# Kernel tuning notes

Hardware: AMD Instinct MI355X
Metric: run time of the kernel (lower is better)

## Reference

```python
import jax, jax.numpy as jnp
import numpy as np

B, T, HID = 2, 2048, 3840
H, KV, D = 16, 8, 256
EPS = 1e-6
WINDOW = 1024
THETA_LOCAL = 10000.0
THETA_GLOBAL = 1000000.0


def _rope_tables(theta, t, d):
    inv_freq = 1.0 / (theta ** (jnp.arange(0, d, 2, dtype=jnp.float32) / d))  # (d/2,)
    ang = jnp.arange(t, dtype=jnp.float32)[:, None] * inv_freq[None, :]        # (T, d/2)
    return jnp.cos(ang), jnp.sin(ang)


def setup_inputs() -> dict:
    key = jax.random.key(0)
    ks = jax.random.split(key, 8)
    x = jax.random.normal(ks[0], (B, T, HID), dtype=jnp.float32)
    wq = jax.random.normal(ks[1], (H * D, HID), dtype=jnp.float32) * 0.02
    wk = jax.random.normal(ks[2], (KV * D, HID), dtype=jnp.float32) * 0.02
    wv = jax.random.normal(ks[3], (KV * D, HID), dtype=jnp.float32) * 0.02
    wo = jax.random.normal(ks[4], (HID, H * D), dtype=jnp.float32) * 0.02
    q_norm_w = 1.0 + jax.random.normal(ks[5], (D,), dtype=jnp.float32) * 0.02
    k_norm_w = 1.0 + jax.random.normal(ks[6], (D,), dtype=jnp.float32) * 0.02
    cos_g, sin_g = _rope_tables(THETA_GLOBAL, T, D)
    cos_l, sin_l = _rope_tables(THETA_LOCAL, T, D)
    # causal + sliding-window(1024) additive float mask, shape (1,1,T,T)
    i = jnp.arange(T)[:, None]
    j = jnp.arange(T)[None, :]
    allowed = (j <= i) & (i - j < WINDOW)
    attention_mask = jnp.where(allowed, 0.0, -1e9).astype(jnp.float32)[None, None]
    return {"x": x, "cos_global": cos_g, "sin_global": sin_g, "cos_local": cos_l,
            "sin_local": sin_l, "attention_mask": attention_mask,
            "wq": wq, "wk": wk, "wv": wv, "wo": wo,
            "q_norm_w": q_norm_w, "k_norm_w": k_norm_w}


def _rms_norm(x, w):
    # add=False variant: x * rsqrt(mean(x^2)+eps) * w, computed in fp32
    norm = jax.lax.rsqrt(jnp.mean(jnp.square(x), axis=-1, keepdims=True) + EPS)
    return x * norm * w


def _apply_rope(x, cos, sin):
    # x: (B, H, T, D); cos/sin: (T, D/2)
    t = x.shape[2]
    c = cos[:t][None, None]
    s = sin[:t][None, None]
    x1, x2 = x[..., : x.shape[-1] // 2], x[..., x.shape[-1] // 2 :]
    return jnp.concatenate([x1 * c - x2 * s, x2 * c + x1 * s], axis=-1)


def reference(x, cos_global, sin_global, cos_local, sin_local, attention_mask,
              wq, wk, wv, wo, q_norm_w, k_norm_w):
    b, t, _ = x.shape
    q = (x @ wq.T).reshape(b, t, H, D).transpose(0, 2, 1, 3)   # (B,H,T,D)
    k = (x @ wk.T).reshape(b, t, KV, D).transpose(0, 2, 1, 3)  # (B,KV,T,D)
    v = (x @ wv.T).reshape(b, t, KV, D).transpose(0, 2, 1, 3)
    q = _rms_norm(q, q_norm_w)
    k = _rms_norm(k, k_norm_w)
    # layer_idx=0 -> sliding-window layer -> local rope
    q = _apply_rope(q, cos_local, sin_local)
    k = _apply_rope(k, cos_local, sin_local)
    rep = H // KV
    k = jnp.repeat(k, rep, axis=1)  # repeat_interleave over head dim
    v = jnp.repeat(v, rep, axis=1)
    scale = 1.0 / jnp.sqrt(jnp.float32(D))
    scores = jnp.einsum("bhqd,bhkd->bhqk", q, k) * scale + attention_mask
    attn = jax.nn.softmax(scores, axis=-1)
    out = jnp.einsum("bhqk,bhkd->bhqd", attn, v)
    out = out.transpose(0, 2, 1, 3).reshape(b, t, H * D)
    return out @ wo.T
```

## Files before the change

### kernel.cpp

```cpp
#include <hip/hip_runtime.h>
#include <hip/hip_bf16.h>

typedef __hip_bfloat16 BF;
typedef __attribute__((ext_vector_type(8))) short short8;
typedef __attribute__((ext_vector_type(4))) float f32x4;

#define DEV __device__ __forceinline__

DEV void gll16(const BF* g, BF* l) {
  __builtin_amdgcn_global_load_lds(
      (const __attribute__((address_space(1))) void*)g,
      (__attribute__((address_space(3))) void*)l, 16, 0, 0);
}

DEV unsigned short bfbits(float f) {
  BF b = __float2bfloat16(f);
  return *reinterpret_cast<unsigned short*>(&b);
}

__global__ void f32_to_bf16_k(const float* __restrict__ in, BF* __restrict__ out, int n4) {
  int i = blockIdx.x * blockDim.x + threadIdx.x;
  if (i >= n4) return;
  const float4 v = ((const float4*)in)[i];
  ((ushort4*)out)[i] = make_ushort4(bfbits(v.x), bfbits(v.y), bfbits(v.z), bfbits(v.w));
}

__global__ void f32_to_bf16_pad_k(const float* __restrict__ in, BF* __restrict__ out, int n4) {
  int i = blockIdx.x * blockDim.x + threadIdx.x;
  if (i >= n4) return;
  const float4 v = ((const float4*)in)[i];
  const int r = i >> 10;
  const int c = i & 1023;
  ((ushort4*)out)[r * 1040 + c] = make_ushort4(bfbits(v.x), bfbits(v.y), bfbits(v.z), bfbits(v.w));
}

#define PHASE(MH, KK, READB, STAGE, TAIL)                                            \
  {                                                                                  \
    short8 af[4];                                                                    \
    const BF* Ap = Ax + (KK)*8192;                                                   \
    _Pragma("unroll") for (int m = 0; m < 4; ++m)                                    \
        af[m] = *(const short8*)&Ap[(wm*128 + (MH)*64 + m*16 + l15) * 32 + rd8];     \
    if (READB) {                                                                     \
      const BF* Bp = Bx + (KK)*8192;                                                 \
      _Pragma("unroll") for (int n = 0; n < 4; ++n)                                  \
          breg[n] = *(const short8*)&Bp[(wn*64 + n*16 + l15) * 32 + rd8];            \
    }                                                                                \
    STAGE                                                                            \
    __builtin_amdgcn_s_barrier();                                                    \
    asm volatile("s_waitcnt lgkmcnt(0)" ::: "memory");                               \
    __builtin_amdgcn_sched_barrier(0);                                               \
    __builtin_amdgcn_s_setprio(1);                                                   \
    _Pragma("unroll") for (int m = 0; m < 4; ++m)                                    \
      _Pragma("unroll") for (int n = 0; n < 4; ++n)                                  \
        acc[(MH)*4 + m][n] =                                                         \
            __builtin_amdgcn_mfma_f32_16x16x32_bf16(af[m], breg[n], acc[(MH)*4+m][n], 0, 0, 0); \
    __builtin_amdgcn_s_setprio(0);                                                   \
    TAIL                                                                             \
    __builtin_amdgcn_s_barrier();                                                    \
  }

template <typename CT>
DEV void gemm256_body(const BF* __restrict__ A, const BF* __restrict__ Bm,
                      CT* __restrict__ C, const int M, const int N, const int K,
                      const int lda, const int ldb) {
  extern __shared__ __align__(16) BF lds[];
  BF* ldsA = lds;
  BF* ldsB = lds + 32768;
  const int ntl = N >> 8;
  const int mtl = M >> 8;
  int mt, nt;
  if (mtl == 16 && ntl == 32) {
    const int x = blockIdx.x & 7;
    const int c = blockIdx.x >> 3;
    mt = ((x >> 2) << 3) + (c >> 3);
    nt = ((x & 3) << 3) + (c & 7);
  } else {
    const int cpx = gridDim.x >> 3;
    const int swzb = (blockIdx.x & 7) * cpx + (blockIdx.x >> 3);
    mt = swzb / ntl;
    nt = swzb % ntl;
  }
  const int m0 = mt << 8, n0 = nt << 8;
  const int tid = threadIdx.x, lane = tid & 63, w = tid >> 6;
  const int l15 = lane & 15, g = lane >> 4;
  const int wm = w >> 2, wn = w & 3;
  const int rd8 = (g ^ ((l15 >> 1) & 3)) << 3;
  const int trow = tid >> 2;
  const int scol = ((lane & 3) ^ ((lane >> 3) & 3)) << 3;
  const BF* aS = A + (size_t)(m0 + trow) * lda + scol;
  const BF* bS = Bm + (size_t)(n0 + trow) * ldb + scol;
  const size_t rstpA = (size_t)128 * lda;
  const size_t rstpB = (size_t)128 * ldb;
  BF* dA = ldsA + w * 512;
  BF* dB = ldsB + w * 512;
  const int NT = K >> 6;

  f32x4 acc[8][4];
#pragma unroll
  for (int m = 0; m < 8; ++m)
#pragma unroll
    for (int n = 0; n < 4; ++n) acc[m][n] = (f32x4){0.f, 0.f, 0.f, 0.f};
  short8 breg[4];

#define STG2(SRC, RST, DST) { gll16((SRC), (DST)); gll16((SRC) + (RST), (DST) + 4096); }

  STG2(aS, rstpA, dA);
  STG2(bS, rstpB, dB);
  STG2(aS + 32, rstpA, dA + 8192);
  STG2(bS + 32, rstpB, dB + 8192);
  STG2(aS + 64, rstpA, dA + 16384);
  STG2(bS + 64, rstpB, dB + 16384);
  asm volatile("s_waitcnt vmcnt(8)" ::: "memory");
  __builtin_amdgcn_sched_barrier(0);
  __builtin_amdgcn_s_barrier();

  for (int t = 0; t < NT; ++t) {
    const int bX = (t & 1) << 14;
    const int bY = bX ^ 16384;
    const BF* Ax = ldsA + bX;
    const BF* Bx = ldsB + bX;
    const int kc1 = (t + 1) << 6, kc2 = (t + 2) << 6;
    const bool s1 = (t + 1 < NT), s2 = (t + 2 < NT);
    PHASE(0, 0, 1, if (s1) STG2(aS + kc1 + 32, rstpA, dA + bY + 8192);, )
    PHASE(1, 0, 0, if (s1) STG2(bS + kc1 + 32, rstpB, dB + bY + 8192);,
          { asm volatile("s_waitcnt vmcnt(8)" ::: "memory");
            __builtin_amdgcn_sched_barrier(0); } )
    PHASE(0, 1, 1, if (s2) STG2(aS + kc2, rstpA, dA + bX);, )
    PHASE(1, 1, 0, if (s2) STG2(bS + kc2, rstpB, dB + bX);,
          if (s2) { asm volatile("s_waitcnt vmcnt(8)" ::: "memory");
                    __builtin_amdgcn_sched_barrier(0); }
          else    { asm volatile("s_waitcnt vmcnt(0)" ::: "memory");
                    __builtin_amdgcn_sched_barrier(0); } )
  }

#pragma unroll
  for (int mi = 0; mi < 8; ++mi) {
    const int gr = m0 + wm * 128 + mi * 16 + g * 4;
#pragma unroll
    for (int n = 0; n < 4; ++n) {
      const int gc = n0 + wn * 64 + n * 16 + l15;
#pragma unroll
      for (int r = 0; r < 4; ++r) {
        const float v = acc[mi][n][r];
        if constexpr (sizeof(CT) == 2)
          C[(size_t)(gr + r) * N + gc] = __float2bfloat16(v);
        else
          C[(size_t)(gr + r) * N + gc] = v;
      }
    }
  }
}

__global__ __launch_bounds__(512, 2) void gemm_qkv(const BF* __restrict__ A,
                                                   const BF* __restrict__ Bm,
                                                   BF* __restrict__ C,
                                                   int M, int N, int K, int lda, int ldb) {
  gemm256_body<BF>(A, Bm, C, M, N, K, lda, ldb);
}
__global__ __launch_bounds__(512, 2) void gemm_out(const BF* __restrict__ A,
                                                   const BF* __restrict__ Bm,
                                                   float* __restrict__ C,
                                                   int M, int N, int K, int lda, int ldb) {
  gemm256_body<float>(A, Bm, C, M, N, K, lda, ldb);
}

__global__ __launch_bounds__(256) void rmsrope(const BF* __restrict__ C1,
                                               BF* __restrict__ Qo, BF* __restrict__ Ko,
                                               const float* __restrict__ cosl,
                                               const float* __restrict__ sinl,
                                               const float* __restrict__ qw,
                                               const float* __restrict__ kw) {
  const int gwid = (blockIdx.x * 256 + threadIdx.x) >> 6;
  const int lane = threadIdx.x & 63;
  const int slot = gwid % 24;
  const int bt = gwid / 24;
  const int b = bt >> 11, t = bt & 2047;
  const BF* src;
  BF* dst;
  const float* wgt;
  if (slot < 16) {
    src = C1 + (size_t)bt * 8192 + slot * 256;
    dst = Qo + ((size_t)(b * 16 + slot) * 2048 + t) * 256;
    wgt = qw;
  } else {
    const int kv = slot - 16;
    src = C1 + (size_t)bt * 8192 + 4096 + kv * 256;
    dst = Ko + ((size_t)(b * 8 + kv) * 2048 + t) * 256;
    wgt = kw;
  }
  const int d2 = lane * 2;
  const ushort2 lo = *(const ushort2*)((const unsigned short*)src + d2);
  const ushort2 hi = *(const ushort2*)((const unsigned short*)src + 128 + d2);
  float x0 = __bfloat162float(*(const BF*)&lo.x);
  float x1 = __bfloat162float(*(const BF*)&lo.y);
  float x2 = __bfloat162float(*(const BF*)&hi.x);
  float x3 = __bfloat162float(*(const BF*)&hi.y);
  float ss = x0 * x0 + x1 * x1 + x2 * x2 + x3 * x3;
#pragma unroll
  for (int mm = 32; mm >= 1; mm >>= 1) ss += __shfl_xor(ss, mm);
  const float nrm = rsqrtf(ss * (1.f / 256.f) + 1e-6f);
  const float2 wlo = *(const float2*)(wgt + d2);
  const float2 whi = *(const float2*)(wgt + 128 + d2);
  x0 *= nrm * wlo.x;
  x1 *= nrm * wlo.y;
  x2 *= nrm * whi.x;
  x3 *= nrm * whi.y;
  const float2 c = *(const float2*)(cosl + t * 128 + d2);
  const float2 s = *(const float2*)(sinl + t * 128 + d2);
  ushort2 olo, ohi;
  olo.x = bfbits(x0 * c.x - x2 * s.x);
  olo.y = bfbits(x1 * c.y - x3 * s.y);
  ohi.x = bfbits(x2 * c.x + x0 * s.x);
  ohi.y = bfbits(x3 * c.y + x1 * s.y);
  *(ushort2*)((unsigned short*)dst + d2) = olo;
  *(ushort2*)((unsigned short*)dst + 128 + d2) = ohi;
}

__global__ void vtrans(const BF* __restrict__ C1, BF* __restrict__ Vt) {
  __shared__ BF tile[32][33];
  const int bz = blockIdx.z;
  const int tt = blockIdx.x;
  const int dt = blockIdx.y;
  const int x = threadIdx.x, y0 = threadIdx.y;
  const int b = bz >> 3, kv = bz & 7;
#pragma unroll
  for (int yy = y0; yy < 32; yy += 8) {
    const int t = tt * 32 + yy, d = dt * 32 + x;
    tile[yy][x] = C1[((size_t)(b * 2048 + t)) * 8192 + 6144 + kv * 256 + d];
  }
  __syncthreads();
#pragma unroll
  for (int yy = y0; yy < 32; yy += 8) {
    const int d = dt * 32 + yy, t = tt * 32 + x;
    Vt[((size_t)bz * 256 + d) * 2048 + t] = tile[x][yy];
  }
}

__global__ __launch_bounds__(256, 2) void attn_fwd(const BF* __restrict__ Q,
                                                   const BF* __restrict__ K,
                                                   const BF* __restrict__ Vt,
                                                   BF* __restrict__ O) {
  __shared__ __align__(16) BF Ks[64 * 256];
  __shared__ __align__(16) BF Vs[256 * 64];
  __shared__ __align__(16) BF Ps[4][1024];
  const int tid = threadIdx.x;
  const int lane = tid & 63;
  const int w = tid >> 6;
  const int l15 = lane & 15;
  const int g = lane >> 4;
  const int qt = blockIdx.x;
  const int bh = blockIdx.y;
  const int b = bh >> 4, h = bh & 15;
  const int kvh = h >> 1;
  const int q0 = qt << 6;
  const BF* Qb = Q + ((size_t)bh * 2048 + q0) * 256;
  const BF* Kb = K + (size_t)(b * 8 + kvh) * 2048 * 256;
  const BF* Vb = Vt + (size_t)(b * 8 + kvh) * 256 * 2048;

  short8 qf[8];
  {
    const BF* qr = Qb + (w * 16 + l15) * 256 + g * 8;
#pragma unroll
    for (int kk = 0; kk < 8; ++kk) qf[kk] = *(const short8*)(qr + kk * 32);
  }
  f32x4 oacc[16];
#pragma unroll
  for (int i = 0; i < 16; ++i) oacc[i] = (f32x4){0.f, 0.f, 0.f, 0.f};
  float m_r[4] = {-1e30f, -1e30f, -1e30f, -1e30f};
  float l_r[4] = {0.f, 0.f, 0.f, 0.f};

  const int kt_lo = (q0 > 1023) ? ((q0 - 1023) >> 6) : 0;
  for (int kt = kt_lo; kt <= qt; ++kt) {
    const int tk = kt << 6;
#pragma unroll
    for (int i = 0; i < 8; ++i) {
      const int li = w * 8 + i;
      {
        const int row = li * 2 + (lane >> 5);
        const int ch = lane & 31;
        gll16(Kb + (size_t)(tk + row) * 256 + ((ch ^ (row & 7)) << 3), Ks + li * 512);
      }
      {
        const int row = li * 8 + (lane >> 3);
        const int ch = lane & 7;
        gll16(Vb + (size_t)row * 2048 + tk + ((ch ^ (row & 7)) << 3), Vs + li * 512);
      }
    }
    __syncthreads();

    f32x4 sa[4];
#pragma unroll
    for (int i2 = 0; i2 < 4; ++i2) sa[i2] = (f32x4){0.f, 0.f, 0.f, 0.f};
#pragma unroll
    for (int kk = 0; kk < 8; ++kk) {
      const int d = kk * 32 + g * 8;
#pragma unroll
      for (int blk = 0; blk < 4; ++blk) {
        const int row = blk * 16 + l15;
        const short8 kf = *(const short8*)&Ks[row * 256 + (d ^ ((row & 7) << 3))];
        sa[blk] = __builtin_amdgcn_mfma_f32_16x16x32_bf16(qf[kk], kf, sa[blk], 0, 0, 0);
      }
    }

    float al4[4];
#pragma unroll
    for (int r = 0; r < 4; ++r) {
      const int qi = q0 + w * 16 + g * 4 + r;
      float pv[4];
      float tmax = -1e30f;
#pragma unroll
      for (int blk = 0; blk < 4; ++blk) {
        const int ki = tk + blk * 16 + l15;
        float sv = sa[blk][r] * 0.0625f;
        const bool ok = (ki <= qi) && (qi - ki < 1024);
        sv = ok ? sv : -1e30f;
        pv[blk] = sv;
        tmax = fmaxf(tmax, sv);
      }
#pragma unroll
      for (int mm = 1; mm < 16; mm <<= 1) tmax = fmaxf(tmax, __shfl_xor(tmax, mm));
      const float mn = fmaxf(m_r[r], tmax);
      const float alpha = __expf(m_r[r] - mn);
      float tsum = 0.f;
#pragma unroll
      for (int blk = 0; blk < 4; ++blk) {
        const float p = __expf(pv[blk] - mn);
        pv[blk] = p;
        tsum += p;
      }
#pragma unroll
      for (int mm = 1; mm < 16; mm <<= 1) tsum += __shfl_xor(tsum, mm);
      l_r[r] = l_r[r] * alpha + tsum;
      m_r[r] = mn;
      al4[r] = alpha;
      const int prow = g * 4 + r;
#pragma unroll
      for (int blk = 0; blk < 4; ++blk) {
        const int col = blk * 16 + l15;
        Ps[w][prow * 64 + (col ^ ((prow & 7) << 3))] = __float2bfloat16(pv[blk]);
      }
    }
#pragma unroll
    for (int db = 0; db < 16; ++db)
#pragma unroll
      for (int r = 0; r < 4; ++r) oacc[db][r] *= al4[r];

#pragma unroll
    for (int kk2 = 0; kk2 < 2; ++kk2) {
      const int k8 = kk2 * 32 + g * 8;
      const short8 pf = *(const short8*)&Ps[w][l15 * 64 + (k8 ^ ((l15 & 7) << 3))];
#pragma unroll
      for (int db = 0; db < 16; ++db) {
        const int vrow = db * 16 + l15;
        const short8 vf = *(const short8*)&Vs[vrow * 64 + (k8 ^ ((vrow & 7) << 3))];
        oacc[db] = __builtin_amdgcn_mfma_f32_16x16x32_bf16(pf, vf, oacc[db], 0, 0, 0);
      }
    }
    __syncthreads();
  }

#pragma unroll
  for (int r = 0; r < 4; ++r) l_r[r] = 1.f / l_r[r];
  const size_t orow0 = (size_t)(b * 2048 + q0 + w * 16 + g * 4);
#pragma unroll
  for (int r = 0; r < 4; ++r) {
    BF* op = O + (orow0 + r) * 4160 + h * 256 + l15;
#pragma unroll
    for (int db = 0; db < 16; ++db) op[db * 16] = __float2bfloat16(oacc[db][r] * l_r[r]);
  }
}

extern "C" void kernel_launch(void* const* d_in, const int* in_sizes, int n_in,
                              void* d_out, int out_size, void* d_ws, size_t ws_size,
                              hipStream_t stream) {
  (void)in_sizes; (void)n_in; (void)out_size;
  const float* x    = (const float*)d_in[0];
  const float* cosl = (const float*)d_in[3];
  const float* sinl = (const float*)d_in[4];
  const float* wq   = (const float*)d_in[6];
  const float* wk   = (const float*)d_in[7];
  const float* wv   = (const float*)d_in[8];
  const float* wo   = (const float*)d_in[9];
  const float* qw   = (const float*)d_in[10];
  const float* kw   = (const float*)d_in[11];
  float* out = (float*)d_out;
  char* ws = (char*)d_ws;
  if (ws_size < 161480704ull) return;

  BF* Wqkv = (BF*)(ws + 0);
  BF* Xbf  = (BF*)(ws + 62914560);
  BF* C1   = (BF*)(ws + 94371840);
  BF* Qb   = (BF*)(ws + 0);
  BF* Kb   = (BF*)(ws + 33554432);
  BF* Vt   = (BF*)(ws + 62914560);
  BF* AO   = (BF*)(ws + 94371840);
  BF* Wo   = (BF*)(ws + 128450560);

  hipFuncSetAttribute(reinterpret_cast<const void*>(gemm_qkv),
                      hipFuncAttributeMaxDynamicSharedMemorySize, 131072);
  hipFuncSetAttribute(reinterpret_cast<const void*>(gemm_out),
                      hipFuncAttributeMaxDynamicSharedMemorySize, 131072);

  auto cvt = [&](const float* src, BF* dst, int n) {
    const int n4 = n >> 2;
    f32_to_bf16_k<<<(n4 + 255) / 256, 256, 0, stream>>>(src, dst, n4);
  };
  cvt(x,  Xbf, 4096 * 3840);
  cvt(wq, Wqkv, 4096 * 3840);
  cvt(wk, Wqkv + 4096 * 3840, 2048 * 3840);
  cvt(wv, Wqkv + 6144 * 3840, 2048 * 3840);

  gemm_qkv<<<512, 512, 131072, stream>>>(Xbf, Wqkv, C1, 4096, 8192, 3840, 3840, 3840);
  rmsrope<<<24576, 256, 0, stream>>>(C1, Qb, Kb, cosl, sinl, qw, kw);
  vtrans<<<dim3(64, 8, 16), dim3(32, 8), 0, stream>>>(C1, Vt);
  {
    const int n4 = (3840 * 4096) >> 2;
    f32_to_bf16_pad_k<<<(n4 + 255) / 256, 256, 0, stream>>>(wo, Wo, n4);
  }
  attn_fwd<<<dim3(32, 32), 256, 0, stream>>>(Qb, Kb, Vt, AO);
  gemm_out<<<240, 512, 131072, stream>>>(AO, Wo, out, 4096, 3840, 4096, 4160, 4160);
}
```

Baseline: 577.4 us.

## Double-buffer LDS fragment registers to overlap ds_reads with MFMA in GEMM

```diff
diff --git a/kernel.cpp b/kernel.cpp
--- a/kernel.cpp
+++ b/kernel.cpp
@@ -34,30 +34,28 @@
   ((ushort4*)out)[r * 1040 + c] = make_ushort4(bfbits(v.x), bfbits(v.y), bfbits(v.z), bfbits(v.w));
 }
 
-#define PHASE(MH, KK, READB, STAGE, TAIL)                                            \
-  {                                                                                  \
-    short8 af[4];                                                                    \
-    const BF* Ap = Ax + (KK)*8192;                                                   \
-    _Pragma("unroll") for (int m = 0; m < 4; ++m)                                    \
-        af[m] = *(const short8*)&Ap[(wm*128 + (MH)*64 + m*16 + l15) * 32 + rd8];     \
-    if (READB) {                                                                     \
-      const BF* Bp = Bx + (KK)*8192;                                                 \
-      _Pragma("unroll") for (int n = 0; n < 4; ++n)                                  \
-          breg[n] = *(const short8*)&Bp[(wn*64 + n*16 + l15) * 32 + rd8];            \
-    }                                                                                \
-    STAGE                                                                            \
-    __builtin_amdgcn_s_barrier();                                                    \
-    asm volatile("s_waitcnt lgkmcnt(0)" ::: "memory");                               \
-    __builtin_amdgcn_sched_barrier(0);                                               \
-    __builtin_amdgcn_s_setprio(1);                                                   \
-    _Pragma("unroll") for (int m = 0; m < 4; ++m)                                    \
-      _Pragma("unroll") for (int n = 0; n < 4; ++n)                                  \
-        acc[(MH)*4 + m][n] =                                                         \
-            __builtin_amdgcn_mfma_f32_16x16x32_bf16(af[m], breg[n], acc[(MH)*4+m][n], 0, 0, 0); \
-    __builtin_amdgcn_s_setprio(0);                                                   \
-    TAIL                                                                             \
-    __builtin_amdgcn_s_barrier();                                                    \
-  }
+
+#define LDA(DST, BASE, MH, KK)                                                        \
+  _Pragma("unroll") for (int m_ = 0; m_ < 4; ++m_)                                    \
+      DST[m_] = *(const short8*)&(BASE)[(KK)*8192 + (wm*128 + (MH)*64 + m_*16 + l15)*32 + rd8];
+#define LDB(DST, BASE, KK)                                                            \
+  _Pragma("unroll") for (int n_ = 0; n_ < 4; ++n_)                                    \
+      DST[n_] = *(const short8*)&(BASE)[(KK)*8192 + (wn*64 + n_*16 + l15)*32 + rd8];
+#define MM(MH, AB, BB)                                                                \
+  __builtin_amdgcn_s_setprio(1);                                                      \
+  _Pragma("unroll") for (int m_ = 0; m_ < 4; ++m_)                                    \
+    _Pragma("unroll") for (int n_ = 0; n_ < 4; ++n_)                                  \
+      acc[(MH)*4 + m_][n_] =                                                          \
+          __builtin_amdgcn_mfma_f32_16x16x32_bf16(AB[m_], BB[n_], acc[(MH)*4 + m_][n_], 0, 0, 0); \
+  __builtin_amdgcn_s_setprio(0);
+#define WAITL(N)                                                                      \
+  asm volatile("s_waitcnt lgkmcnt(" #N ")" ::: "memory");                             \
+  __builtin_amdgcn_sched_barrier(0);
+#define WAITV(N)                                                                      \
+  asm volatile("s_waitcnt vmcnt(" #N ")" ::: "memory");                               \
+  __builtin_amdgcn_sched_barrier(0);
+#define BAR() __builtin_amdgcn_s_barrier();
+#define STG2(SRC, RST, DST) { gll16((SRC), (DST)); gll16((SRC) + (RST), (DST) + 4096); }
 
 template <typename CT>
 DEV void gemm256_body(const BF* __restrict__ A, const BF* __restrict__ Bm,
@@ -100,9 +98,7 @@
   for (int m = 0; m < 8; ++m)
 #pragma unroll
     for (int n = 0; n < 4; ++n) acc[m][n] = (f32x4){0.f, 0.f, 0.f, 0.f};
-  short8 breg[4];
-
-#define STG2(SRC, RST, DST) { gll16((SRC), (DST)); gll16((SRC) + (RST), (DST) + 4096); }
+  short8 afA[4], afB[4], bfA[4], bfB[4];
 
   STG2(aS, rstpA, dA);
   STG2(bS, rstpB, dB);
@@ -110,27 +106,51 @@
   STG2(bS + 32, rstpB, dB + 8192);
   STG2(aS + 64, rstpA, dA + 16384);
   STG2(bS + 64, rstpB, dB + 16384);
-  asm volatile("s_waitcnt vmcnt(8)" ::: "memory");
-  __builtin_amdgcn_sched_barrier(0);
-  __builtin_amdgcn_s_barrier();
+  WAITV(4)
+  BAR()
+  LDA(afA, ldsA, 0, 0)
+  LDB(bfA, ldsB, 0)
 
   for (int t = 0; t < NT; ++t) {
     const int bX = (t & 1) << 14;
     const int bY = bX ^ 16384;
     const BF* Ax = ldsA + bX;
     const BF* Bx = ldsB + bX;
+    const BF* Ay = ldsA + bY;
+    const BF* By = ldsB + bY;
     const int kc1 = (t + 1) << 6, kc2 = (t + 2) << 6;
     const bool s1 = (t + 1 < NT), s2 = (t + 2 < NT);
-    PHASE(0, 0, 1, if (s1) STG2(aS + kc1 + 32, rstpA, dA + bY + 8192);, )
-    PHASE(1, 0, 0, if (s1) STG2(bS + kc1 + 32, rstpB, dB + bY + 8192);,
-          { asm volatile("s_waitcnt vmcnt(8)" ::: "memory");
-            __builtin_amdgcn_sched_barrier(0); } )
-    PHASE(0, 1, 1, if (s2) STG2(aS + kc2, rstpA, dA + bX);, )
-    PHASE(1, 1, 0, if (s2) STG2(bS + kc2, rstpB, dB + bX);,
-          if (s2) { asm volatile("s_waitcnt vmcnt(8)" ::: "memory");
-                    __builtin_amdgcn_sched_barrier(0); }
-          else    { asm volatile("s_waitcnt vmcnt(0)" ::: "memory");
-                    __builtin_amdgcn_sched_barrier(0); } )
+
+    LDA(afB, Ax, 1, 0)
+    if (s1) STG2(aS + kc1 + 32, rstpA, dA + bY + 8192);
+    BAR()
+    WAITL(4)
+    MM(0, afA, bfA)
+    BAR()
+
+    LDA(afA, Ax, 0, 1)
+    LDB(bfB, Bx, 1)
+    if (s1) STG2(bS + kc1 + 32, rstpB, dB + bY + 8192);
+    BAR()
+    WAITL(8)
+    MM(1, afB, bfA)
+    BAR()
+
+    LDA(afB, Ax, 1, 1)
+    if (s2) STG2(aS + kc2, rstpA, dA + bX);
+    BAR()
+    WAITL(4)
+    MM(0, afA, bfB)
+    if (s2) { WAITV(6) } else { WAITV(0) }
+    BAR()
+
+    if (s1) { LDA(afA, Ay, 0, 0) LDB(bfA, By, 0) }
+    if (s2) STG2(bS + kc2, rstpB, dB + bX);
+    BAR()
+    if (s1) { WAITL(8) } else { WAITL(0) }
+    MM(1, afB, bfB)
+    if (s2) { WAITV(4) } else { WAITV(0) }
+    BAR()
   }
 
 #pragma unroll
```

After: 582.7 us. Within noise of the previous version (+0.9%).

## Share K/V tiles across GQA head pair in attention and fuse input conversions

Applied to the files above, without the earlier changes.

```diff
diff --git a/kernel.cpp b/kernel.cpp
--- a/kernel.cpp
+++ b/kernel.cpp
@@ -18,20 +18,32 @@
   return *reinterpret_cast<unsigned short*>(&b);
 }
 
-__global__ void f32_to_bf16_k(const float* __restrict__ in, BF* __restrict__ out, int n4) {
-  int i = blockIdx.x * blockDim.x + threadIdx.x;
-  if (i >= n4) return;
-  const float4 v = ((const float4*)in)[i];
-  ((ushort4*)out)[i] = make_ushort4(bfbits(v.x), bfbits(v.y), bfbits(v.z), bfbits(v.w));
+DEV ushort4 cvt4(const float4 v) {
+  return make_ushort4(bfbits(v.x), bfbits(v.y), bfbits(v.z), bfbits(v.w));
+}
+
+__global__ void cvt_fused(const float* __restrict__ x, const float* __restrict__ wq,
+                          const float* __restrict__ wk, const float* __restrict__ wv,
+                          BF* __restrict__ Xbf, BF* __restrict__ Wqkv) {
+  const int stride = gridDim.x * blockDim.x;
+  for (int i = blockIdx.x * blockDim.x + threadIdx.x; i < 11796480; i += stride) {
+    const float* src;
+    ushort4* dst;
+    int off;
+    if (i < 3932160)      { src = x;  off = i;           dst = (ushort4*)Xbf; }
+    else if (i < 7864320) { src = wq; off = i - 3932160; dst = (ushort4*)Wqkv; }
+    else if (i < 9830400) { src = wk; off = i - 7864320; dst = (ushort4*)(Wqkv + 4096 * 3840); }
+    else                  { src = wv; off = i - 9830400; dst = (ushort4*)(Wqkv + 6144 * 3840); }
+    dst[off] = cvt4(((const float4*)src)[off]);
+  }
 }
 
 __global__ void f32_to_bf16_pad_k(const float* __restrict__ in, BF* __restrict__ out, int n4) {
   int i = blockIdx.x * blockDim.x + threadIdx.x;
   if (i >= n4) return;
-  const float4 v = ((const float4*)in)[i];
   const int r = i >> 10;
   const int c = i & 1023;
-  ((ushort4*)out)[r * 1040 + c] = make_ushort4(bfbits(v.x), bfbits(v.y), bfbits(v.z), bfbits(v.w));
+  ((ushort4*)out)[r * 1040 + c] = cvt4(((const float4*)in)[i]);
 }
 
 #define PHASE(MH, KK, READB, STAGE, TAIL)                                            \
@@ -59,6 +71,8 @@
     __builtin_amdgcn_s_barrier();                                                    \
   }
 
+#define STG2(SRC, RST, DST) { gll16((SRC), (DST)); gll16((SRC) + (RST), (DST) + 4096); }
+
 template <typename CT>
 DEV void gemm256_body(const BF* __restrict__ A, const BF* __restrict__ Bm,
                       CT* __restrict__ C, const int M, const int N, const int K,
@@ -101,8 +115,6 @@
 #pragma unroll
     for (int n = 0; n < 4; ++n) acc[m][n] = (f32x4){0.f, 0.f, 0.f, 0.f};
   short8 breg[4];
-
-#define STG2(SRC, RST, DST) { gll16((SRC), (DST)); gll16((SRC) + (RST), (DST) + 4096); }
 
   STG2(aS, rstpA, dA);
   STG2(bS, rstpB, dB);
@@ -236,30 +248,32 @@
   }
 }
 
-__global__ __launch_bounds__(256, 2) void attn_fwd(const BF* __restrict__ Q,
+__global__ __launch_bounds__(512, 1) void attn_fwd(const BF* __restrict__ Q,
                                                    const BF* __restrict__ K,
                                                    const BF* __restrict__ Vt,
                                                    BF* __restrict__ O) {
   __shared__ __align__(16) BF Ks[64 * 256];
   __shared__ __align__(16) BF Vs[256 * 64];
-  __shared__ __align__(16) BF Ps[4][1024];
+  __shared__ __align__(16) BF Ps[8][1024];
   const int tid = threadIdx.x;
   const int lane = tid & 63;
   const int w = tid >> 6;
+  const int wh = w >> 2;
+  const int wq = w & 3;
   const int l15 = lane & 15;
   const int g = lane >> 4;
   const int qt = blockIdx.x;
-  const int bh = blockIdx.y;
-  const int b = bh >> 4, h = bh & 15;
-  const int kvh = h >> 1;
+  const int bp = blockIdx.y;
+  const int b = bp >> 3, kvh = bp & 7;
+  const int h = kvh * 2 + wh;
   const int q0 = qt << 6;
-  const BF* Qb = Q + ((size_t)bh * 2048 + q0) * 256;
+  const BF* Qb = Q + ((size_t)(b * 16 + h) * 2048 + q0) * 256;
   const BF* Kb = K + (size_t)(b * 8 + kvh) * 2048 * 256;
   const BF* Vb = Vt + (size_t)(b * 8 + kvh) * 256 * 2048;
 
   short8 qf[8];
   {
-    const BF* qr = Qb + (w * 16 + l15) * 256 + g * 8;
+    const BF* qr = Qb + (wq * 16 + l15) * 256 + g * 8;
 #pragma unroll
     for (int kk = 0; kk < 8; ++kk) qf[kk] = *(const short8*)(qr + kk * 32);
   }
@@ -273,8 +287,8 @@
   for (int kt = kt_lo; kt <= qt; ++kt) {
     const int tk = kt << 6;
 #pragma unroll
-    for (int i = 0; i < 8; ++i) {
-      const int li = w * 8 + i;
+    for (int i = 0; i < 4; ++i) {
+      const int li = w * 4 + i;
       {
         const int row = li * 2 + (lane >> 5);
         const int ch = lane & 31;
@@ -305,7 +319,7 @@
     float al4[4];
 #pragma unroll
     for (int r = 0; r < 4; ++r) {
-      const int qi = q0 + w * 16 + g * 4 + r;
+      const int qi = q0 + wq * 16 + g * 4 + r;
       float pv[4];
       float tmax = -1e30f;
 #pragma unroll
@@ -361,7 +375,7 @@
 
 #pragma unroll
   for (int r = 0; r < 4; ++r) l_r[r] = 1.f / l_r[r];
-  const size_t orow0 = (size_t)(b * 2048 + q0 + w * 16 + g * 4);
+  const size_t orow0 = (size_t)(b * 2048 + q0 + wq * 16 + g * 4);
 #pragma unroll
   for (int r = 0; r < 4; ++r) {
     BF* op = O + (orow0 + r) * 4160 + h * 256 + l15;
@@ -401,14 +415,7 @@
   hipFuncSetAttribute(reinterpret_cast<const void*>(gemm_out),
                       hipFuncAttributeMaxDynamicSharedMemorySize, 131072);
 
-  auto cvt = [&](const float* src, BF* dst, int n) {
-    const int n4 = n >> 2;
-    f32_to_bf16_k<<<(n4 + 255) / 256, 256, 0, stream>>>(src, dst, n4);
-  };
-  cvt(x,  Xbf, 4096 * 3840);
-  cvt(wq, Wqkv, 4096 * 3840);
-  cvt(wk, Wqkv + 4096 * 3840, 2048 * 3840);
-  cvt(wv, Wqkv + 6144 * 3840, 2048 * 3840);
+  cvt_fused<<<2048, 256, 0, stream>>>(x, wq, wk, wv, Xbf, Wqkv);
 
   gemm_qkv<<<512, 512, 131072, stream>>>(Xbf, Wqkv, C1, 4096, 8192, 3840, 3840, 3840);
   rmsrope<<<24576, 256, 0, stream>>>(C1, Qb, Kb, cosl, sinl, qw, kw);
@@ -417,6 +424,6 @@
     const int n4 = (3840 * 4096) >> 2;
     f32_to_bf16_pad_k<<<(n4 + 255) / 256, 256, 0, stream>>>(wo, Wo, n4);
   }
-  attn_fwd<<<dim3(32, 32), 256, 0, stream>>>(Qb, Kb, Vt, AO);
+  attn_fwd<<<dim3(32, 16), 512, 0, stream>>>(Qb, Kb, Vt, AO);
   gemm_out<<<240, 512, 131072, stream>>>(AO, Wo, out, 4096, 3840, 4096, 4160, 4160);
 }
```

After: 567.5 us. No clear change (-1.7%).
